# Kernel optimization log

Hardware: AMD Instinct MI355X
Metric: run time of the kernel (lower is better)

## Reference

```python
import jax, jax.numpy as jnp
import numpy as np

DIM = 384
WIN = 7
HEADS = 12
N = WIN * WIN
B_ = 4096
NW = 64


def _relative_position_index(ws: int) -> np.ndarray:
    coords = np.stack(np.meshgrid(np.arange(ws), np.arange(ws), indexing='ij'))  # (2, ws, ws)
    flat = coords.reshape(2, -1)  # (2, N)
    rel = flat[:, :, None] - flat[:, None, :]  # (2, N, N)
    rel = rel.transpose(1, 2, 0).copy()  # (N, N, 2)
    rel[:, :, 0] += ws - 1
    rel[:, :, 1] += ws - 1
    rel[:, :, 0] *= 2 * ws - 1
    return rel.sum(-1).astype(np.int32)  # (N, N)


def setup_inputs() -> dict:
    key = jax.random.key(0)
    ks = jax.random.split(key, 6)
    x = jax.random.normal(ks[0], (B_, N, DIM), dtype=jnp.float32)
    mask = jnp.zeros((NW, N, N), dtype=jnp.float32)
    bias_table = 0.02 * jax.random.normal(ks[1], ((2 * WIN - 1) ** 2, HEADS), dtype=jnp.float32)
    qkv_w = jax.random.normal(ks[2], (3 * DIM, DIM), dtype=jnp.float32) / np.sqrt(DIM)
    qkv_b = jnp.zeros((3 * DIM,), dtype=jnp.float32)
    proj_w = jax.random.normal(ks[3], (DIM, DIM), dtype=jnp.float32) / np.sqrt(DIM)
    proj_b = jnp.zeros((DIM,), dtype=jnp.float32)
    rel_index = jnp.asarray(_relative_position_index(WIN))  # (N, N) int32
    return {"x": x, "mask": mask, "bias_table": bias_table, "qkv_w": qkv_w,
            "qkv_b": qkv_b, "proj_w": proj_w, "proj_b": proj_b, "rel_index": rel_index}


def reference(x, mask, bias_table, qkv_w, qkv_b, proj_w, proj_b, rel_index):
    Bw, n, c = x.shape
    h = bias_table.shape[1]
    d = c // h
    scale = d ** (-0.5)
    # qkv projection: (Bw, n, 3, h, d)
    qkv = (x @ qkv_w.T + qkv_b).reshape(Bw, n, 3, h, d)
    qkv = jnp.transpose(qkv, (2, 0, 3, 1, 4))  # (3, Bw, h, n, d)
    q, k, v = qkv[0], qkv[1], qkv[2]
    attn = jnp.einsum('bhqd,bhkd->bhqk', q * scale, k)  # (Bw, h, n, n)
    bias = bias_table[rel_index]  # (n, n, h)
    attn = attn + jnp.transpose(bias, (2, 0, 1))[None]  # broadcast over Bw
    nW = mask.shape[0]
    attn = attn.reshape(Bw // nW, nW, h, n, n) + mask[None, :, None]
    attn = attn.reshape(Bw, h, n, n)
    attn = jax.nn.softmax(attn, axis=-1)
    out = jnp.einsum('bhqk,bhkd->bhqd', attn, v)  # (Bw, h, n, d)
    out = jnp.transpose(out, (0, 2, 1, 3)).reshape(Bw, n, c)
    return out @ proj_w.T + proj_b
```

## Files before the change

### kernel.cpp

```cpp
#include <hip/hip_runtime.h>
#include <hip/hip_bf16.h>

#define DIM   384
#define NWIN  49
#define HEADS 12
#define SCALE 0.17677669529663687f

typedef unsigned short ushort;
using bf16x8 = __attribute__((ext_vector_type(8))) short;
using u16x4  = __attribute__((ext_vector_type(4))) ushort;
using f32x4  = __attribute__((ext_vector_type(4))) float;

__device__ __forceinline__ ushort f2bf(float f) {
  unsigned u = __float_as_uint(f);
  u += 0x7fff + ((u >> 16) & 1);
  return (ushort)(u >> 16);
}

typedef __attribute__((address_space(1))) const void gas_void;
typedef __attribute__((address_space(3))) void las_void;

__device__ __forceinline__ void gload16(const ushort* g, ushort* l) {
  __builtin_amdgcn_global_load_lds((gas_void*)g, (las_void*)l, 16, 0, 0);
}

__global__ void prep_kernel(const float* __restrict__ qkv_w, const float* __restrict__ proj_w,
                            const float* __restrict__ bias_table, const int* __restrict__ rel_index,
                            const float* __restrict__ mask, const float* __restrict__ qkv_b,
                            ushort* __restrict__ wqb, ushort* __restrict__ wpb,
                            float* __restrict__ qbF, float* __restrict__ bmF) {
  int i0 = blockIdx.x * 256 + threadIdx.x;
  int stride = gridDim.x * 256;
  for (int i = i0; i < 1152 * 384; i += stride) {
    float v = qkv_w[i];
    if (i < 384 * 384) v *= SCALE;
    wqb[i] = f2bf(v);
  }
  for (int i = i0; i < 384 * 384; i += stride) wpb[i] = f2bf(proj_w[i]);
  for (int i = i0; i < 1152; i += stride) qbF[i] = qkv_b[i] * (i < 384 ? SCALE : 1.f);
  for (int i = i0; i < 64 * HEADS * 4 * 4 * 64 * 4; i += stride) {
    int r = i & 3, lane = (i >> 2) & 63, kt = (i >> 8) & 3, wq = (i >> 10) & 3;
    int hw = i >> 12;
    int h = hw % HEADS, wdx = hw / HEADS;
    int q = wq * 16 + (lane >> 4) * 4 + r;
    int key = kt * 16 + (lane & 15);
    float v;
    if (q < NWIN)
      v = (key < NWIN) ? bias_table[rel_index[q * NWIN + key] * HEADS + h]
                         + mask[wdx * (NWIN * NWIN) + q * NWIN + key]
                       : -3.0e38f;
    else
      v = 0.f;
    bmF[i] = v;
  }
}

__global__ __launch_bounds__(256) void qkv_gemm_kernel(
    const float* __restrict__ x, const float* __restrict__ qbF,
    const ushort* __restrict__ wqb,
    ushort* __restrict__ qg, ushort* __restrict__ kg, ushort* __restrict__ vg)
{
  extern __shared__ ushort smA[];
  ushort* lA = smA;
  ushort* lB = smA + 16384;

  const int blk = blockIdx.x;
  const int bM = blk / 9, bN = blk - bM * 9;
  const int m0 = bM * 128, n0 = bN * 128;
  const int which = bN / 3;
  ushort* outw = which == 0 ? qg : (which == 1 ? kg : vg);
  const int tid = threadIdx.x;
  const int w = tid >> 6, l = tid & 63;
  const int c = l & 15, g = l >> 4;
  const int wm = w >> 1, wn = w & 1;

  auto stageA = [&](int kc, int buf) {
    #pragma unroll
    for (int s = 0; s < 4; ++s) {
      int i = s * 256 + tid;
      int row = i >> 3, gc = i & 7;
      const float4* src = (const float4*)(x + (size_t)(m0 + row) * DIM + kc * 64 + gc * 8);
      float4 f0 = src[0], f1 = src[1];
      ushort tmp[8] = { f2bf(f0.x), f2bf(f0.y), f2bf(f0.z), f2bf(f0.w),
                        f2bf(f1.x), f2bf(f1.y), f2bf(f1.z), f2bf(f1.w) };
      *(bf16x8*)&lA[buf * 8192 + row * 64 + ((gc ^ (row & 7)) << 3)] = *(bf16x8*)tmp;
    }
  };
  auto stageB = [&](int kc, int buf) {
    #pragma unroll
    for (int s = 0; s < 4; ++s) {
      int i = s * 256 + tid;
      int row = i >> 3, gc = i & 7;
      gload16(wqb + (size_t)(n0 + row) * DIM + kc * 64 + ((gc ^ (row & 7)) << 3),
              lB + buf * 8192 + i * 8);
    }
  };

  f32x4 acc[4][4] = {};
  stageA(0, 0); stageB(0, 0);
  stageA(1, 1); stageB(1, 1);
  __syncthreads();

  for (int kc = 0; kc < 6; ++kc) {
    const ushort* A = lA + (kc & 1) * 8192;
    const ushort* B = lB + (kc & 1) * 8192;
    #pragma unroll
    for (int kk = 0; kk < 2; ++kk) {
      int swz = ((kk * 4 + g) ^ (c & 7)) << 3;
      bf16x8 af[4], bfr[4];
      #pragma unroll
      for (int mt = 0; mt < 4; ++mt)
        af[mt] = *(const bf16x8*)&A[(wm * 64 + mt * 16 + c) * 64 + swz];
      #pragma unroll
      for (int nt = 0; nt < 4; ++nt)
        bfr[nt] = *(const bf16x8*)&B[(wn * 64 + nt * 16 + c) * 64 + swz];
      #pragma unroll
      for (int mt = 0; mt < 4; ++mt)
        #pragma unroll
        for (int nt = 0; nt < 4; ++nt)
          acc[mt][nt] = __builtin_amdgcn_mfma_f32_16x16x32_bf16(af[mt], bfr[nt], acc[mt][nt], 0, 0, 0);
    }
    __syncthreads();
    if (kc + 2 < 6) { stageA(kc + 2, kc & 1); stageB(kc + 2, kc & 1); }
  }

  #pragma unroll
  for (int nt = 0; nt < 4; ++nt) {
    int n = n0 + wn * 64 + nt * 16 + c;
    int h = (n - which * 384) >> 5;
    int d = n & 31;
    float qb_ = qbF[n];
    #pragma unroll
    for (int mt = 0; mt < 4; ++mt) {
      #pragma unroll
      for (int r = 0; r < 4; ++r) {
        int tok = m0 + wm * 64 + mt * 16 + g * 4 + r;
        int win = tok / 49;
        int tk = tok - win * 49;
        outw[((size_t)(win * HEADS + h) * NWIN + tk) * 32 + d] = f2bf(acc[mt][nt][r] + qb_);
      }
    }
  }
}

#define VSTR 68
__global__ __launch_bounds__(256) void attn_kernel(
    const ushort* __restrict__ kg, const ushort* __restrict__ vg,
    const float* __restrict__ bmF, ushort* __restrict__ qg)
{
  __shared__ ushort vts[4][32 * VSTR];
  __shared__ ushort pbs[4][16 * 36];

  const int tid = threadIdx.x;
  const int w = tid >> 6, l = tid & 63;
  const int c = l & 15, g = l >> 4;
  const int task = blockIdx.x * 4 + w;
  const int win = task / 12, h = task - win * 12;
  const int wdx = win & 63;
  const float LOG2E = 1.4426950408889634f;

  const size_t sb = (size_t)(win * HEADS + h) * (NWIN * 32);
  ushort* qslice = qg + sb;
  const ushort* kb = kg + sb;
  const ushort* vb = vg + sb;
  ushort* vt = vts[w];
  ushort* pb = pbs[w];

  bf16x8 qf[4], kf[4];
  #pragma unroll
  for (int t = 0; t < 4; ++t) {
    qf[t] = *(const bf16x8*)(qslice + (t * 16 + c) * 32 + g * 8);
    kf[t] = *(const bf16x8*)(kb + (t * 16 + c) * 32 + g * 8);
  }
  #pragma unroll
  for (int it = 0; it < 25; ++it) {
    int i = it * 64 + l;
    if (i < NWIN * 32) vt[(i & 31) * VSTR + (i >> 5)] = vb[i];
  }
  for (int i = l; i < 32 * 15; i += 64) {
    int d = i / 15, t = NWIN + (i - d * 15);
    vt[d * VSTR + t] = 0;
  }

  const float* bmBase = bmF + (size_t)((wdx * HEADS + h) * 4) * 1024 + l * 4;

  #pragma unroll
  for (int qt = 0; qt < 4; ++qt) {
    f32x4 sacc[4] = {};
    #pragma unroll
    for (int kt = 0; kt < 4; ++kt)
      sacc[kt] = __builtin_amdgcn_mfma_f32_16x16x32_bf16(qf[qt], kf[kt], sacc[kt], 0, 0, 0);
    const f32x4* bw4 = (const f32x4*)(bmBase + qt * 1024);
    float p[4][4];
    {
      f32x4 b0 = bw4[0], b1 = bw4[64], b2 = bw4[128], b3 = bw4[192];
      #pragma unroll
      for (int r = 0; r < 4; ++r) {
        float s0 = sacc[0][r] + b0[r], s1 = sacc[1][r] + b1[r];
        float s2 = sacc[2][r] + b2[r], s3 = sacc[3][r] + b3[r];
        float mx = fmaxf(fmaxf(s0, s1), fmaxf(s2, s3));
        mx = fmaxf(mx, __shfl_xor(mx, 1, 64));
        mx = fmaxf(mx, __shfl_xor(mx, 2, 64));
        mx = fmaxf(mx, __shfl_xor(mx, 4, 64));
        mx = fmaxf(mx, __shfl_xor(mx, 8, 64));
        float p0 = __builtin_exp2f((s0 - mx) * LOG2E);
        float p1 = __builtin_exp2f((s1 - mx) * LOG2E);
        float p2 = __builtin_exp2f((s2 - mx) * LOG2E);
        float p3 = __builtin_exp2f((s3 - mx) * LOG2E);
        float sum = p0 + p1 + p2 + p3;
        sum += __shfl_xor(sum, 1, 64);
        sum += __shfl_xor(sum, 2, 64);
        sum += __shfl_xor(sum, 4, 64);
        sum += __shfl_xor(sum, 8, 64);
        float inv = 1.0f / sum;
        p[0][r] = p0 * inv; p[1][r] = p1 * inv; p[2][r] = p2 * inv; p[3][r] = p3 * inv;
      }
    }
    f32x4 pacc[2] = {};
    #pragma unroll
    for (int kkh = 0; kkh < 2; ++kkh) {
      #pragma unroll
      for (int t = 0; t < 2; ++t) {
        int kt = kkh * 2 + t;
        #pragma unroll
        for (int r = 0; r < 4; ++r)
          pb[(g * 4 + r) * 36 + t * 16 + c] = f2bf(p[kt][r]);
      }
      bf16x8 ap = *(const bf16x8*)&pb[c * 36 + g * 8];
      #pragma unroll
      for (int dt = 0; dt < 2; ++dt) {
        bf16x8 bv = *(const bf16x8*)&vt[(dt * 16 + c) * VSTR + kkh * 32 + g * 8];
        pacc[dt] = __builtin_amdgcn_mfma_f32_16x16x32_bf16(ap, bv, pacc[dt], 0, 0, 0);
      }
    }
    #pragma unroll
    for (int dt = 0; dt < 2; ++dt) {
      #pragma unroll
      for (int rr = 0; rr < 4; ++rr) {
        int tok = qt * 16 + g * 4 + rr;
        if (tok < NWIN)
          qslice[tok * 32 + dt * 16 + c] = f2bf(pacc[dt][rr]);
      }
    }
  }
}

__global__ __launch_bounds__(256, 2) void proj_kernel(
    const ushort* __restrict__ ao, const ushort* __restrict__ wpb,
    const float* __restrict__ proj_b, float* __restrict__ out)
{
  extern __shared__ ushort sm3[];
  ushort* lA = sm3;
  ushort* lB = sm3 + 16384;

  const int blk = blockIdx.x;
  const int bM = blk / 3, bN = blk - bM * 3;
  const int m0 = bM * 128, n0 = bN * 128;
  const int tid = threadIdx.x;
  const int w = tid >> 6, l = tid & 63;
  const int c = l & 15, g = l >> 4;
  const int wm = w >> 1, wn = w & 1;

  auto stageA = [&](int kc, int buf) {
    #pragma unroll
    for (int s = 0; s < 4; ++s) {
      int i = s * 256 + tid;
      int row = i >> 3, gc = i & 7;
      int tok = m0 + row;
      int win = tok / 49;
      int tk = tok - win * 49;
      int sg = gc ^ (row & 7);
      int kfull = kc * 64 + sg * 8;
      gload16(ao + ((size_t)(win * HEADS + (kfull >> 5)) * NWIN + tk) * 32 + (kfull & 31),
              lA + buf * 8192 + i * 8);
    }
  };
  auto stageB = [&](int kc, int buf) {
    #pragma unroll
    for (int s = 0; s < 4; ++s) {
      int i = s * 256 + tid;
      int row = i >> 3, gc = i & 7;
      gload16(wpb + (size_t)(n0 + row) * DIM + kc * 64 + ((gc ^ (row & 7)) << 3),
              lB + buf * 8192 + i * 8);
    }
  };

  f32x4 acc[4][4] = {};
  stageA(0, 0); stageB(0, 0);
  stageA(1, 1); stageB(1, 1);
  __syncthreads();

  for (int kc = 0; kc < 6; ++kc) {
    const ushort* A = lA + (kc & 1) * 8192;
    const ushort* B = lB + (kc & 1) * 8192;
    #pragma unroll
    for (int kk = 0; kk < 2; ++kk) {
      int swz = ((kk * 4 + g) ^ (c & 7)) << 3;
      bf16x8 af[4], bfr[4];
      #pragma unroll
      for (int mt = 0; mt < 4; ++mt)
        af[mt] = *(const bf16x8*)&A[(wm * 64 + mt * 16 + c) * 64 + swz];
      #pragma unroll
      for (int nt = 0; nt < 4; ++nt)
        bfr[nt] = *(const bf16x8*)&B[(wn * 64 + nt * 16 + c) * 64 + swz];
      #pragma unroll
      for (int mt = 0; mt < 4; ++mt)
        #pragma unroll
        for (int nt = 0; nt < 4; ++nt)
          acc[mt][nt] = __builtin_amdgcn_mfma_f32_16x16x32_bf16(af[mt], bfr[nt], acc[mt][nt], 0, 0, 0);
    }
    __syncthreads();
    if (kc + 2 < 6) { stageA(kc + 2, kc & 1); stageB(kc + 2, kc & 1); }
  }

  #pragma unroll
  for (int nt = 0; nt < 4; ++nt) {
    int col = n0 + wn * 64 + nt * 16 + c;
    float pb = proj_b[col];
    #pragma unroll
    for (int mt = 0; mt < 4; ++mt) {
      #pragma unroll
      for (int r = 0; r < 4; ++r) {
        int row = m0 + wm * 64 + mt * 16 + g * 4 + r;
        out[(size_t)row * DIM + col] = acc[mt][nt][r] + pb;
      }
    }
  }
}

#define FWB_OFF 0
#define FQS_OFF 24576
#define FKS_OFF 29696
#define FVT_OFF 34816
#define FAO_OFF 39424
#define FSMEM_US 77056

__global__ __launch_bounds__(512, 2) void winattn_fused(
    const float* __restrict__ x, const float* __restrict__ qbF,
    const float* __restrict__ proj_b, const ushort* __restrict__ wqb,
    const ushort* __restrict__ wpb, const float* __restrict__ bmF,
    float* __restrict__ out)
{
  extern __shared__ ushort smem[];
  ushort* wb = smem + FWB_OFF;
  ushort* ao = smem + FAO_OFF;

  const int blk = blockIdx.x;
  const int tid = threadIdx.x;
  const int w = tid >> 6, l = tid & 63;
  const int c = l & 15, g = l >> 4;
  const int wm = w >> 1, wn = w & 1;
  const int win = w >> 2, wq = w & 3;
  const float LOG2E = 1.4426950408889634f;

  ushort* qsw = smem + FQS_OFF + win * 2560;
  ushort* ksw = smem + FKS_OFF + win * 2560;
  ushort* vtw = smem + FVT_OFF + win * 2304;
  ushort* psw = qsw;

  auto stage_qkv = [&](int h, int kc, int buf) {
    #pragma unroll
    for (int s = 0; s < 3; ++s) {
      int i = s * 512 + tid;
      int n = i >> 4, g16 = i & 15;
      int grow = (n >> 5) * 384 + h * 32 + (n & 31);
      int sg = (g16 & 8) | ((g16 & 7) ^ (n & 7));
      gload16(wqb + (size_t)grow * DIM + kc * 128 + (sg << 3), wb + buf * 12288 + i * 8);
    }
  };
  auto stage_proj = [&](int nb, int kc, int buf) {
    #pragma unroll
    for (int s = 0; s < 3; ++s) {
      int i = s * 512 + tid;
      int n = i >> 4, g16 = i & 15;
      int grow = nb * 96 + n;
      int sg = (g16 & 8) | ((g16 & 7) ^ (n & 7));
      gload16(wpb + (size_t)grow * DIM + kc * 128 + (sg << 3), wb + buf * 12288 + i * 8);
    }
  };

  bf16x8 areg[2][12] = {};
  auto compute_qkv = [&](int kcC, int buf, f32x4 (&acc)[2][3]) {
    const ushort* wcb = wb + buf * 12288;
    #pragma unroll
    for (int kk = 0; kk < 4; ++kk) {
      int sB = ((kk * 4 + g) ^ (c & 7)) << 3;
      #pragma unroll
      for (int nt = 0; nt < 3; ++nt) {
        int n = (wn * 3 + nt) * 16 + c;
        bf16x8 bb = *(const bf16x8*)&wcb[n * 128 + sB];
        acc[0][nt] = __builtin_amdgcn_mfma_f32_16x16x32_bf16(areg[0][kcC * 4 + kk], bb, acc[0][nt], 0, 0, 0);
        acc[1][nt] = __builtin_amdgcn_mfma_f32_16x16x32_bf16(areg[1][kcC * 4 + kk], bb, acc[1][nt], 0, 0, 0);
      }
    }
  };
  auto compute_proj = [&](int kcC, int buf, f32x4 (&acc)[2][3]) {
    const ushort* wcb = wb + buf * 12288;
    int r0 = wm * 32 + c;      if (r0 >= 98) r0 -= 64;
    int r1 = wm * 32 + 16 + c; if (r1 >= 98) r1 -= 64;
    #pragma unroll
    for (int kk = 0; kk < 4; ++kk) {
      int p = kcC * 16 + kk * 4 + g;
      int sw = (p ^ (c & 7)) << 3;
      bf16x8 a0 = *(const bf16x8*)&ao[r0 * 384 + sw];
      bf16x8 a1 = *(const bf16x8*)&ao[r1 * 384 + sw];
      int sB = ((kk * 4 + g) ^ (c & 7)) << 3;
      #pragma unroll
      for (int nt = 0; nt < 3; ++nt) {
        int n = (wn * 3 + nt) * 16 + c;
        bf16x8 bb = *(const bf16x8*)&wcb[n * 128 + sB];
        acc[0][nt] = __builtin_amdgcn_mfma_f32_16x16x32_bf16(a0, bb, acc[0][nt], 0, 0, 0);
        acc[1][nt] = __builtin_amdgcn_mfma_f32_16x16x32_bf16(a1, bb, acc[1][nt], 0, 0, 0);
      }
    }
  };

  stage_qkv(0, 0, 0);
  stage_qkv(0, 1, 1);
  {
    const float* xb = x + (size_t)blk * (2 * NWIN * DIM);
    for (int i = tid; i < 9408; i += 512) {
      float4 f = ((const float4*)xb)[i];
      int row = i / 96, c4 = i - row * 96;
      int k = c4 * 4;
      int gr = k >> 3;
      u16x4 v4 = { f2bf(f.x), f2bf(f.y), f2bf(f.z), f2bf(f.w) };
      *(u16x4*)&ao[row * 384 + ((gr ^ (row & 7)) << 3) + (k & 7)] = v4;
    }
  }
  __syncthreads();
  #pragma unroll
  for (int mt = 0; mt < 2; ++mt) {
    int row = wm * 32 + mt * 16 + c;
    int wi = row >> 6, tok = row & 63;
    if (tok < NWIN) {
      int ar = wi * 49 + tok;
      #pragma unroll
      for (int kg = 0; kg < 12; ++kg)
        areg[mt][kg] = *(const bf16x8*)&ao[ar * 384 + (((kg * 4 + g) ^ (ar & 7)) << 3)];
    }
  }

  for (int h = 0; h < HEADS; ++h) {
    f32x4 acc[2][3] = {};
    const int par = h & 1;
    compute_qkv(0, par, acc);
    __syncthreads();
    stage_qkv(h, 2, par);
    compute_qkv(1, par ^ 1, acc);
    __syncthreads();
    if (h < 11) stage_qkv(h + 1, 0, par ^ 1); else stage_proj(0, 0, par ^ 1);
    compute_qkv(2, par, acc);
    __syncthreads();
    if (h < 11) stage_qkv(h + 1, 1, par); else stage_proj(0, 1, par);
    {
      int winE = wm >> 1;
      ushort* qsE = smem + FQS_OFF + winE * 2560;
      ushort* ksE = smem + FKS_OFF + winE * 2560;
      ushort* vtE = smem + FVT_OFF + winE * 2304;
      #pragma unroll
      for (int nt = 0; nt < 3; ++nt) {
        int gnt = wn * 3 + nt;
        int which = gnt >> 1;
        int d = (gnt & 1) * 16 + c;
        float qb_ = qbF[which * 384 + h * 32 + d];
        #pragma unroll
        for (int mt = 0; mt < 2; ++mt) {
          #pragma unroll
          for (int r = 0; r < 4; ++r) {
            int tok = (wm & 1) * 32 + mt * 16 + g * 4 + r;
            float v = acc[mt][nt][r] + qb_;
            if (which == 0)      qsE[tok * 40 + d] = f2bf(v);
            else if (which == 1) ksE[tok * 40 + d] = f2bf(v);
            else                 vtE[d * 72 + tok] = f2bf(v);
          }
        }
      }
    }
    __syncthreads();

    const int wdx = ((blk << 1) + win) & 63;
    const f32x4* bw4 = (const f32x4*)(bmF + ((((size_t)(wdx * HEADS + h)) * 4 + wq) * 4 * 64 + l) * 4);
    f32x4 bmv[4];
    #pragma unroll
    for (int kt = 0; kt < 4; ++kt) bmv[kt] = bw4[kt * 64];

    f32x4 sacc[4] = {};
    {
      bf16x8 aq = *(const bf16x8*)&qsw[(wq * 16 + c) * 40 + g * 8];
      #pragma unroll
      for (int kt = 0; kt < 4; ++kt) {
        bf16x8 bk = *(const bf16x8*)&ksw[(kt * 16 + c) * 40 + g * 8];
        sacc[kt] = __builtin_amdgcn_mfma_f32_16x16x32_bf16(aq, bk, sacc[kt], 0, 0, 0);
      }
    }
    float p[4][4];
    #pragma unroll
    for (int r = 0; r < 4; ++r) {
      float s0 = sacc[0][r] + bmv[0][r], s1 = sacc[1][r] + bmv[1][r];
      float s2 = sacc[2][r] + bmv[2][r], s3 = sacc[3][r] + bmv[3][r];
      float mx = fmaxf(fmaxf(s0, s1), fmaxf(s2, s3));
      mx = fmaxf(mx, __shfl_xor(mx, 1, 64));
      mx = fmaxf(mx, __shfl_xor(mx, 2, 64));
      mx = fmaxf(mx, __shfl_xor(mx, 4, 64));
      mx = fmaxf(mx, __shfl_xor(mx, 8, 64));
      float p0 = __builtin_exp2f((s0 - mx) * LOG2E);
      float p1 = __builtin_exp2f((s1 - mx) * LOG2E);
      float p2 = __builtin_exp2f((s2 - mx) * LOG2E);
      float p3 = __builtin_exp2f((s3 - mx) * LOG2E);
      float sum = p0 + p1 + p2 + p3;
      sum += __shfl_xor(sum, 1, 64);
      sum += __shfl_xor(sum, 2, 64);
      sum += __shfl_xor(sum, 4, 64);
      sum += __shfl_xor(sum, 8, 64);
      float inv = 1.0f / sum;
      p[0][r] = p0 * inv; p[1][r] = p1 * inv; p[2][r] = p2 * inv; p[3][r] = p3 * inv;
    }
    f32x4 pacc2[2] = {};
    #pragma unroll
    for (int kkh = 0; kkh < 2; ++kkh) {
      #pragma unroll
      for (int t = 0; t < 2; ++t) {
        int kt = kkh * 2 + t;
        #pragma unroll
        for (int r = 0; r < 4; ++r)
          psw[(wq * 16 + g * 4 + r) * 40 + t * 16 + c] = f2bf(p[kt][r]);
      }
      bf16x8 ap = *(const bf16x8*)&psw[(wq * 16 + c) * 40 + g * 8];
      #pragma unroll
      for (int dt = 0; dt < 2; ++dt) {
        bf16x8 bv = *(const bf16x8*)&vtw[(dt * 16 + c) * 72 + kkh * 32 + g * 8];
        pacc2[dt] = __builtin_amdgcn_mfma_f32_16x16x32_bf16(ap, bv, pacc2[dt], 0, 0, 0);
      }
    }
    #pragma unroll
    for (int dt = 0; dt < 2; ++dt) {
      int gr0 = h * 4 + dt * 2 + (c >> 3);
      #pragma unroll
      for (int rr = 0; rr < 4; ++rr) {
        int tok = wq * 16 + g * 4 + rr;
        int row0 = win * 49 + tok;
        if (tok < NWIN)
          ao[row0 * 384 + (((gr0 ^ (row0 & 7)) << 3) | (c & 7))] = f2bf(pacc2[dt][rr]);
      }
    }
    __syncthreads();
  }

  __syncthreads();
  for (int nb = 0; nb < 4; ++nb) {
    f32x4 acc[2][3] = {};
    const int pb0 = (nb * 3) & 1;
    compute_proj(0, pb0, acc);
    __syncthreads();
    stage_proj(nb, 2, pb0);
    compute_proj(1, pb0 ^ 1, acc);
    __syncthreads();
    if (nb < 3) stage_proj(nb + 1, 0, pb0 ^ 1);
    compute_proj(2, pb0, acc);
    __syncthreads();
    if (nb < 3) stage_proj(nb + 1, 1, pb0);
    #pragma unroll
    for (int nt = 0; nt < 3; ++nt) {
      int col = nb * 96 + (wn * 3 + nt) * 16 + c;
      float pb = proj_b[col];
      #pragma unroll
      for (int mt = 0; mt < 2; ++mt) {
        #pragma unroll
        for (int r = 0; r < 4; ++r) {
          int mrow = wm * 32 + mt * 16 + g * 4 + r;
          if (mrow < 98) {
            int wi = mrow >= NWIN;
            int tok = mrow - (wi ? NWIN : 0);
            out[((size_t)((blk << 1) + wi) * NWIN + tok) * DIM + col] = acc[mt][nt][r] + pb;
          }
        }
      }
    }
  }
}

extern "C" void kernel_launch(void* const* d_in, const int* in_sizes, int n_in,
                              void* d_out, int out_size, void* d_ws, size_t ws_size,
                              hipStream_t stream) {
  const float* x          = (const float*)d_in[0];
  const float* mask       = (const float*)d_in[1];
  const float* bias_table = (const float*)d_in[2];
  const float* qkv_w      = (const float*)d_in[3];
  const float* qkv_b      = (const float*)d_in[4];
  const float* proj_w     = (const float*)d_in[5];
  const float* proj_b     = (const float*)d_in[6];
  const int*   rel_index  = (const int*)d_in[7];
  float* out = (float*)d_out;

  ushort* wqb = (ushort*)d_ws;
  ushort* wpb = (ushort*)((char*)d_ws + 884736);
  float*  qbF = (float*)((char*)d_ws + 1179648);
  float*  bmF = (float*)((char*)d_ws + 1184256);
  ushort* qg  = (ushort*)((char*)d_ws + 13767168);
  ushort* kg  = (ushort*)((char*)d_ws + 167907840);
  ushort* vg  = (ushort*)((char*)d_ws + 322048512);
  const size_t NEED = 476189184ull;

  prep_kernel<<<1024, 256, 0, stream>>>(qkv_w, proj_w, bias_table, rel_index, mask, qkv_b,
                                        wqb, wpb, qbF, bmF);

  if (ws_size >= NEED) {
    hipFuncSetAttribute((const void*)qkv_gemm_kernel,
                        hipFuncAttributeMaxDynamicSharedMemorySize, 65536);
    qkv_gemm_kernel<<<14112, 256, 65536, stream>>>(x, qbF, wqb, qg, kg, vg);
    attn_kernel<<<12288, 256, 0, stream>>>(kg, vg, bmF, qg);
    hipFuncSetAttribute((const void*)proj_kernel,
                        hipFuncAttributeMaxDynamicSharedMemorySize, 65536);
    proj_kernel<<<4704, 256, 65536, stream>>>(qg, wpb, proj_b, out);
  } else {
    hipFuncSetAttribute((const void*)winattn_fused,
                        hipFuncAttributeMaxDynamicSharedMemorySize, FSMEM_US * 2);
    winattn_fused<<<2048, 512, FSMEM_US * 2, stream>>>(x, qbF, proj_b, wqb, wpb, bmF, out);
  }
}
```

Measured before the change: 929.7 us.

## Pre-convert x to bf16 in a separate pass and remap GEMM blocks per XCD

Adds a kernel that converts the fp32 input to bf16 once, and a new QKV GEMM that stages bf16 A tiles directly instead of converting fp32 inside each of the nine N-column blocks. This removes redundant fp32 reads and conversions across the column tiles. The price is an extra full pass writing and reading a bf16 copy of x, plus more workspace. Block indices in the QKV and projection GEMMs are also remapped so consecutive M panels land on the same XCD, aiming at better L2 reuse of the A rows.

```diff
diff --git a/kernel.cpp b/kernel.cpp
--- a/kernel.cpp
+++ b/kernel.cpp
@@ -55,6 +55,101 @@
   }
 }
 
+__global__ __launch_bounds__(256) void x2bf_kernel(const float* __restrict__ x,
+                                                   ushort* __restrict__ xbf) {
+  size_t i = (size_t)blockIdx.x * 256 + threadIdx.x;
+  float4 f = ((const float4*)x)[i];
+  u16x4 v4 = { f2bf(f.x), f2bf(f.y), f2bf(f.z), f2bf(f.w) };
+  ((u16x4*)xbf)[i] = v4;
+}
+
+__global__ __launch_bounds__(256) void qkv_gemm_bf16_kernel(
+    const ushort* __restrict__ xbf, const float* __restrict__ qbF,
+    const ushort* __restrict__ wqb,
+    ushort* __restrict__ qg, ushort* __restrict__ kg, ushort* __restrict__ vg)
+{
+  extern __shared__ ushort smA[];
+  ushort* lA = smA;
+  ushort* lB = smA + 16384;
+
+  const int hw = blockIdx.x;
+  const int xcd = hw & 7, slot = hw >> 3;
+  const int pan = slot / 9, bN = slot - pan * 9;
+  const int bM = (pan << 3) + xcd;
+  const int m0 = bM * 128, n0 = bN * 128;
+  const int which = bN / 3;
+  ushort* outw = which == 0 ? qg : (which == 1 ? kg : vg);
+  const int tid = threadIdx.x;
+  const int w = tid >> 6, l = tid & 63;
+  const int c = l & 15, g = l >> 4;
+  const int wm = w >> 1, wn = w & 1;
+
+  auto stageA = [&](int kc, int buf) {
+    #pragma unroll
+    for (int s = 0; s < 4; ++s) {
+      int i = s * 256 + tid;
+      int row = i >> 3, gc = i & 7;
+      bf16x8 vx = *(const bf16x8*)(xbf + (size_t)(m0 + row) * DIM + kc * 64 + gc * 8);
+      *(bf16x8*)&lA[buf * 8192 + row * 64 + ((gc ^ (row & 7)) << 3)] = vx;
+    }
+  };
+  auto stageB = [&](int kc, int buf) {
+    #pragma unroll
+    for (int s = 0; s < 4; ++s) {
+      int i = s * 256 + tid;
+      int row = i >> 3, gc = i & 7;
+      gload16(wqb + (size_t)(n0 + row) * DIM + kc * 64 + ((gc ^ (row & 7)) << 3),
+              lB + buf * 8192 + i * 8);
+    }
+  };
+
+  f32x4 acc[4][4] = {};
+  stageA(0, 0); stageB(0, 0);
+  stageA(1, 1); stageB(1, 1);
+  __syncthreads();
+
+  for (int kc = 0; kc < 6; ++kc) {
+    const ushort* A = lA + (kc & 1) * 8192;
+    const ushort* B = lB + (kc & 1) * 8192;
+    #pragma unroll
+    for (int kk = 0; kk < 2; ++kk) {
+      int swz = ((kk * 4 + g) ^ (c & 7)) << 3;
+      bf16x8 af[4], bfr[4];
+      #pragma unroll
+      for (int mt = 0; mt < 4; ++mt)
+        af[mt] = *(const bf16x8*)&A[(wm * 64 + mt * 16 + c) * 64 + swz];
+      #pragma unroll
+      for (int nt = 0; nt < 4; ++nt)
+        bfr[nt] = *(const bf16x8*)&B[(wn * 64 + nt * 16 + c) * 64 + swz];
+      #pragma unroll
+      for (int mt = 0; mt < 4; ++mt)
+        #pragma unroll
+        for (int nt = 0; nt < 4; ++nt)
+          acc[mt][nt] = __builtin_amdgcn_mfma_f32_16x16x32_bf16(af[mt], bfr[nt], acc[mt][nt], 0, 0, 0);
+    }
+    __syncthreads();
+    if (kc + 2 < 6) { stageA(kc + 2, kc & 1); stageB(kc + 2, kc & 1); }
+  }
+
+  #pragma unroll
+  for (int nt = 0; nt < 4; ++nt) {
+    int n = n0 + wn * 64 + nt * 16 + c;
+    int h = (n - which * 384) >> 5;
+    int d = n & 31;
+    float qb_ = qbF[n];
+    #pragma unroll
+    for (int mt = 0; mt < 4; ++mt) {
+      #pragma unroll
+      for (int r = 0; r < 4; ++r) {
+        int tok = m0 + wm * 64 + mt * 16 + g * 4 + r;
+        int win = tok / 49;
+        int tk = tok - win * 49;
+        outw[((size_t)(win * HEADS + h) * NWIN + tk) * 32 + d] = f2bf(acc[mt][nt][r] + qb_);
+      }
+    }
+  }
+}
+
 __global__ __launch_bounds__(256) void qkv_gemm_kernel(
     const float* __restrict__ x, const float* __restrict__ qbF,
     const ushort* __restrict__ wqb,
@@ -64,8 +159,10 @@
   ushort* lA = smA;
   ushort* lB = smA + 16384;
 
-  const int blk = blockIdx.x;
-  const int bM = blk / 9, bN = blk - bM * 9;
+  const int hw = blockIdx.x;
+  const int xcd = hw & 7, slot = hw >> 3;
+  const int pan = slot / 9, bN = slot - pan * 9;
+  const int bM = (pan << 3) + xcd;
   const int m0 = bM * 128, n0 = bN * 128;
   const int which = bN / 3;
   ushort* outw = which == 0 ? qg : (which == 1 ? kg : vg);
@@ -253,8 +350,10 @@
   ushort* lA = sm3;
   ushort* lB = sm3 + 16384;
 
-  const int blk = blockIdx.x;
-  const int bM = blk / 3, bN = blk - bM * 3;
+  const int hw = blockIdx.x;
+  const int xcd = hw & 7, slot = hw >> 3;
+  const int pan = slot / 3, bN = slot - pan * 3;
+  const int bM = (pan << 3) + xcd;
   const int m0 = bM * 128, n0 = bN * 128;
   const int tid = threadIdx.x;
   const int w = tid >> 6, l = tid & 63;
@@ -600,12 +699,23 @@
   ushort* qg  = (ushort*)((char*)d_ws + 13767168);
   ushort* kg  = (ushort*)((char*)d_ws + 167907840);
   ushort* vg  = (ushort*)((char*)d_ws + 322048512);
-  const size_t NEED = 476189184ull;
+  ushort* xbf = (ushort*)((char*)d_ws + 476189184);
+  const size_t NEED1 = 630329856ull;
+  const size_t NEED2 = 476189184ull;
 
   prep_kernel<<<1024, 256, 0, stream>>>(qkv_w, proj_w, bias_table, rel_index, mask, qkv_b,
                                         wqb, wpb, qbF, bmF);
 
-  if (ws_size >= NEED) {
+  if (ws_size >= NEED1) {
+    x2bf_kernel<<<75264, 256, 0, stream>>>(x, xbf);
+    hipFuncSetAttribute((const void*)qkv_gemm_bf16_kernel,
+                        hipFuncAttributeMaxDynamicSharedMemorySize, 65536);
+    qkv_gemm_bf16_kernel<<<14112, 256, 65536, stream>>>(xbf, qbF, wqb, qg, kg, vg);
+    attn_kernel<<<12288, 256, 0, stream>>>(kg, vg, bmF, qg);
+    hipFuncSetAttribute((const void*)proj_kernel,
+                        hipFuncAttributeMaxDynamicSharedMemorySize, 65536);
+    proj_kernel<<<4704, 256, 65536, stream>>>(qg, wpb, proj_b, out);
+  } else if (ws_size >= NEED2) {
     hipFuncSetAttribute((const void*)qkv_gemm_kernel,
                         hipFuncAttributeMaxDynamicSharedMemorySize, 65536);
     qkv_gemm_kernel<<<14112, 256, 65536, stream>>>(x, qbF, wqb, qg, kg, vg);
```

After: 794.6 us. 1.17x faster.
